# Kernel optimization log

Measured on AMD Instinct MI355X. Metric: run time of the kernel, lower is better.

## Reference

```python
import jax, jax.numpy as jnp
import numpy as np
from jax import lax

EPS = 1e-8


def setup_inputs() -> dict:
    key = jax.random.key(0)
    k1, k2, k3, k4, k5 = jax.random.split(key, 5)
    b, c_in, c_out, h, w_sp, k, z = 8, 256, 256, 128, 128, 3, 512
    return {
        "x": jax.random.normal(k1, (b, c_in, h, w_sp), dtype=jnp.float32),
        "w": jax.random.normal(k2, (b, z), dtype=jnp.float32),
        "weight": jax.random.normal(k3, (c_out, c_in, k, k), dtype=jnp.float32),
        "affine_w": jax.random.normal(k4, (c_in, z), dtype=jnp.float32) * 0.02,
        "affine_b": jax.random.normal(k5, (c_in,), dtype=jnp.float32) * 0.02,
    }


def reference(x, w, weight, affine_w, affine_b):
    # style: [b, c_in] -> broadcast over (out_ch, kh, kw); +1 as in StyleGAN2
    style = w @ affine_w.T + affine_b + 1.0                      # [b, c_in]
    wgt = weight[None] * style[:, None, :, None, None]           # [b, O, I, kh, kw]
    # demodulation
    denom = lax.rsqrt(jnp.sum(wgt * wgt, axis=(2, 3, 4)) + EPS)  # [b, O]
    wgt = wgt * denom[:, :, None, None, None]

    # per-sample conv (equivalent to groups=b grouped conv), 'same' padding
    def conv_one(xi, wi):
        # xi: [I, H, W], wi: [O, I, kh, kw]
        return lax.conv_general_dilated(
            xi[None], wi, window_strides=(1, 1), padding="SAME",
            dimension_numbers=("NCHW", "OIHW", "NCHW"))[0]

    return jax.vmap(conv_one)(x, wgt)                            # [b, O, H, W]
```

## Files before the change

kernel.cpp:

```cpp
#include <hip/hip_runtime.h>
#include <hip/hip_bf16.h>

#define EPS 1e-8f

using short8 = __attribute__((ext_vector_type(8))) short;
using f32x16 = __attribute__((ext_vector_type(16))) float;
typedef unsigned short u16;

#define BARRIER() do { __builtin_amdgcn_s_barrier(); \
                       asm volatile("" ::: "memory"); } while (0)
#define LGKM0() asm volatile("s_waitcnt lgkmcnt(0)" ::: "memory")

__device__ __forceinline__ u16 f2bf(float f) {
    union { float f; unsigned u; } v; v.f = f;
    unsigned u = v.u;
    return (u16)((u + 0x7FFFu + ((u >> 16) & 1u)) >> 16);
}

__global__ void style_kernel(const float* __restrict__ w,
                             const float* __restrict__ affine_w,
                             const float* __restrict__ affine_b,
                             float* __restrict__ style) {
    int b = blockIdx.x;
    int i = threadIdx.x;
    __shared__ float wb[512];
    for (int z = threadIdx.x; z < 512; z += 256) wb[z] = w[b * 512 + z];
    __syncthreads();
    const float* aw = affine_w + i * 512;
    float acc = 0.f;
#pragma unroll 4
    for (int z = 0; z < 512; z += 4) {
        float4 a4 = *reinterpret_cast<const float4*>(aw + z);
        acc += a4.x * wb[z] + a4.y * wb[z + 1] + a4.z * wb[z + 2] + a4.w * wb[z + 3];
    }
    style[b * 256 + i] = acc + affine_b[i] + 1.0f;
}

__global__ void modw_kernel(const float* __restrict__ weight,
                            const float* __restrict__ style,
                            u16* __restrict__ wgt) {
    int b = blockIdx.x >> 8;
    int o = blockIdx.x & 255;
    int ic = threadIdx.x;
    float s = style[b * 256 + ic];
    const float* wp = weight + (size_t)(o * 256 + ic) * 9;
    float m[9];
    float ss = 0.f;
#pragma unroll
    for (int t = 0; t < 9; ++t) { m[t] = wp[t] * s; ss += m[t] * m[t]; }
#pragma unroll
    for (int off = 32; off > 0; off >>= 1) ss += __shfl_down(ss, off);
    __shared__ float part[4];
    int lane = threadIdx.x & 63, wid = threadIdx.x >> 6;
    if (lane == 0) part[wid] = ss;
    __syncthreads();
    float denom = rsqrtf(part[0] + part[1] + part[2] + part[3] + EPS);
    int g = ic >> 3, j = ic & 7;
#pragma unroll
    for (int t = 0; t < 9; ++t) {
        size_t idx = ((((size_t)(b * 9 + t) * 32 + g) * 256 + o) << 3) + j;
        wgt[idx] = f2bf(m[t] * denom);
    }
}

__global__ __launch_bounds__(256, 2) void conv_kernel(
    const float* __restrict__ x,
    const u16* __restrict__ wgt,
    float* __restrict__ out) {

    __shared__ __align__(16) u16 Xs[2][4][4][130][8];

    int bid = blockIdx.x;
    int swz = (bid & 7) * 128 + (bid >> 3);
    int ht = swz & 63, ot = (swz >> 6) & 1, b = swz >> 7;
    int h0 = ht * 2;

    int tid = threadIdx.x, lane = tid & 63, wid = tid >> 6;
    int wm = wid >> 1, wr = wid & 1;
    int l31 = lane & 31, lh = lane >> 5;

    int hr = h0 + wid - 1;
    bool hValid = ((unsigned)hr < 128u);
    int hc = hValid ? hr : 0;

    const u16* aBase = wgt + ((size_t)(b * 9) * 32 * 256 +
                              (size_t)(lh * 256 + ot * 128 + wm * 64 + l31)) * 8;
    const float* xBase = x + ((size_t)(b * 256) * 128 + hc) * 128;

    auto loadA = [&](short8 dst[2][2], int c, int t) {
#pragma unroll
        for (int kk = 0; kk < 2; ++kk)
#pragma unroll
            for (int mi = 0; mi < 2; ++mi)
                dst[kk][mi] = *reinterpret_cast<const short8*>(
                    aBase + (size_t)(((t * 32) + c * 4 + kk * 2) * 256 + mi * 32) * 8);
    };
    auto issueX = [&](float* dst, int c1, int bt) {
        int g = bt >> 1, half = bt & 1;
        const float* sp = xBase + (size_t)(c1 * 32 + g * 8) * 16384 + half * 64 + lane;
#pragma unroll
        for (int j = 0; j < 8; ++j) dst[j] = sp[(size_t)j * 16384];
    };
    auto writeX = [&](const float* src, int bt, int bx) {
        int g = bt >> 1, half = bt & 1;
        union { u16 u[8]; short8 v; } pk;
#pragma unroll
        for (int j = 0; j < 8; ++j) {
            __hip_bfloat16 hb = __float2bfloat16(src[j]);
            pk.u[j] = reinterpret_cast<u16&>(hb);
        }
        *reinterpret_cast<short8*>(&Xs[bx][wid][g][1 + half * 64 + lane][0]) = pk.v;
    };

    {
        short8 z = {0, 0, 0, 0, 0, 0, 0, 0};
        short8* p0 = reinterpret_cast<short8*>(&Xs[0][0][0][0][0]);
        for (int i = tid; i < 4160; i += 256) p0[i] = z;
    }
    __syncthreads();

    short8 afC[2][2], afN[2][2];
    if (hValid) {
        float xg0[8][8];
#pragma unroll
        for (int bt = 0; bt < 8; ++bt) issueX(xg0[bt], 0, bt);
#pragma unroll
        for (int bt = 0; bt < 8; ++bt) writeX(xg0[bt], bt, 0);
    }
    loadA(afC, 0, 0);
    LGKM0();
    BARRIER();

    f32x16 acc[2][4] = {};
    float xg[2][8];

    for (int c = 0; c < 8; ++c) {
        int buf = c & 1;
        bool stage = (c < 7) && hValid;
#pragma unroll
        for (int t = 0; t < 9; ++t) {
            bool lastTap = (c == 7 && t == 8);
            if (!lastTap)
                loadA(afN, t < 8 ? c : c + 1, t < 8 ? t + 1 : 0);
            if (stage) {
                if (t >= 2) writeX(xg[t & 1], t - 2, buf ^ 1);
                if (t < 8)  issueX(xg[t & 1], c + 1, t);
                if (t == 8) writeX(xg[1], 7, buf ^ 1);
            }

            int kh = t / 3, kw = t - kh * 3;
            short8 bx8[2][4];
#pragma unroll
            for (int kk = 0; kk < 2; ++kk)
#pragma unroll
                for (int ni = 0; ni < 4; ++ni)
                    bx8[kk][ni] = *reinterpret_cast<const short8*>(
                        &Xs[buf][wr + kh][kk * 2 + lh][ni * 32 + l31 + kw][0]);
            __builtin_amdgcn_s_setprio(1);
#pragma unroll
            for (int mi = 0; mi < 2; ++mi)
#pragma unroll
                for (int ni = 0; ni < 4; ++ni)
#pragma unroll
                    for (int kk = 0; kk < 2; ++kk)
                        acc[mi][ni] = __builtin_amdgcn_mfma_f32_32x32x16_bf16(
                            afC[kk][mi], bx8[kk][ni], acc[mi][ni], 0, 0, 0);
            __builtin_amdgcn_s_setprio(0);

            if (!lastTap) {
#pragma unroll
                for (int k2 = 0; k2 < 2; ++k2)
#pragma unroll
                    for (int mi = 0; mi < 2; ++mi)
                        afC[k2][mi] = afN[k2][mi];
            }
        }
        if (c < 7) { LGKM0(); BARRIER(); }
    }

    int h = h0 + wr;
#pragma unroll
    for (int mi = 0; mi < 2; ++mi) {
        int ob = ot * 128 + wm * 64 + mi * 32 + 4 * lh;
#pragma unroll
        for (int ni = 0; ni < 4; ++ni) {
            int w_ = ni * 32 + l31;
#pragma unroll
            for (int reg = 0; reg < 16; ++reg) {
                int o = ob + (reg & 3) + 8 * (reg >> 2);
                out[(((size_t)(b * 256 + o) * 128 + h) * 128) + w_] = acc[mi][ni][reg];
            }
        }
    }
}

extern "C" void kernel_launch(void* const* d_in, const int* in_sizes, int n_in,
                              void* d_out, int out_size, void* d_ws, size_t ws_size,
                              hipStream_t stream) {
    const float* x        = (const float*)d_in[0];
    const float* w        = (const float*)d_in[1];
    const float* weight   = (const float*)d_in[2];
    const float* affine_w = (const float*)d_in[3];
    const float* affine_b = (const float*)d_in[4];
    float* out = (float*)d_out;

    float* style = (float*)d_ws;
    u16* wgt = (u16*)((char*)d_ws + 8192);

    style_kernel<<<8, 256, 0, stream>>>(w, affine_w, affine_b, style);
    modw_kernel<<<2048, 256, 0, stream>>>(weight, style, wgt);
    conv_kernel<<<1024, 256, 0, stream>>>(x, wgt, out);
}
```

Baseline: 182.9 us.

## Retile conv blocks to one output row across all 256 output channels

Each block now computes one spatial row for all 256 output channels, where before it computed two rows for 128 channels. The LDS input halo shrinks from 4 rows to 3, and that halo is shared across all output channels. This cuts redundant x loads and fp32-to-bf16 conversions, since the old ot split loaded the same input twice. In exchange, each modulated weight fragment is reused across only one row instead of two, which doubles weight traffic per output, and boundary rows now need per-row validity checks during staging.

```diff
diff --git a/kernel.cpp b/kernel.cpp
--- a/kernel.cpp
+++ b/kernel.cpp
@@ -68,24 +68,17 @@
     const u16* __restrict__ wgt,
     float* __restrict__ out) {
 
-    __shared__ __align__(16) u16 Xs[2][4][4][130][8];
+    __shared__ __align__(16) u16 Xs[2][3][4][130][8];
 
     int bid = blockIdx.x;
     int swz = (bid & 7) * 128 + (bid >> 3);
-    int ht = swz & 63, ot = (swz >> 6) & 1, b = swz >> 7;
-    int h0 = ht * 2;
+    int h = swz & 127, b = swz >> 7;
 
     int tid = threadIdx.x, lane = tid & 63, wid = tid >> 6;
-    int wm = wid >> 1, wr = wid & 1;
     int l31 = lane & 31, lh = lane >> 5;
 
-    int hr = h0 + wid - 1;
-    bool hValid = ((unsigned)hr < 128u);
-    int hc = hValid ? hr : 0;
-
     const u16* aBase = wgt + ((size_t)(b * 9) * 32 * 256 +
-                              (size_t)(lh * 256 + ot * 128 + wm * 64 + l31)) * 8;
-    const float* xBase = x + ((size_t)(b * 256) * 128 + hc) * 128;
+                              (size_t)(lh * 256 + wid * 64 + l31)) * 8;
 
     auto loadA = [&](short8 dst[2][2], int c, int t) {
 #pragma unroll
@@ -95,37 +88,44 @@
                 dst[kk][mi] = *reinterpret_cast<const short8*>(
                     aBase + (size_t)(((t * 32) + c * 4 + kk * 2) * 256 + mi * 32) * 8);
     };
-    auto issueX = [&](float* dst, int c1, int bt) {
-        int g = bt >> 1, half = bt & 1;
-        const float* sp = xBase + (size_t)(c1 * 32 + g * 8) * 16384 + half * 64 + lane;
-#pragma unroll
-        for (int j = 0; j < 8; ++j) dst[j] = sp[(size_t)j * 16384];
+    auto issueX = [&](float* dst, int c1, int u) {
+        int row = u >> 3, g = (u >> 1) & 3, half = u & 1;
+        int hr = h + row - 1;
+        if ((unsigned)hr < 128u) {
+            const float* sp = x + (((size_t)(b * 256 + c1 * 32 + g * 8)) * 128 + hr) * 128 +
+                              half * 64 + lane;
+#pragma unroll
+            for (int j = 0; j < 8; ++j) dst[j] = sp[(size_t)j * 16384];
+        }
     };
-    auto writeX = [&](const float* src, int bt, int bx) {
-        int g = bt >> 1, half = bt & 1;
-        union { u16 u[8]; short8 v; } pk;
-#pragma unroll
-        for (int j = 0; j < 8; ++j) {
-            __hip_bfloat16 hb = __float2bfloat16(src[j]);
-            pk.u[j] = reinterpret_cast<u16&>(hb);
-        }
-        *reinterpret_cast<short8*>(&Xs[bx][wid][g][1 + half * 64 + lane][0]) = pk.v;
+    auto writeX = [&](const float* src, int u, int bx) {
+        int row = u >> 3, g = (u >> 1) & 3, half = u & 1;
+        int hr = h + row - 1;
+        if ((unsigned)hr < 128u) {
+            union { u16 u[8]; short8 v; } pk;
+#pragma unroll
+            for (int j = 0; j < 8; ++j) {
+                __hip_bfloat16 hb = __float2bfloat16(src[j]);
+                pk.u[j] = reinterpret_cast<u16&>(hb);
+            }
+            *reinterpret_cast<short8*>(&Xs[bx][row][g][1 + half * 64 + lane][0]) = pk.v;
+        }
     };
 
     {
         short8 z = {0, 0, 0, 0, 0, 0, 0, 0};
         short8* p0 = reinterpret_cast<short8*>(&Xs[0][0][0][0][0]);
-        for (int i = tid; i < 4160; i += 256) p0[i] = z;
+        for (int i = tid; i < 3120; i += 256) p0[i] = z;
     }
     __syncthreads();
 
     short8 afC[2][2], afN[2][2];
-    if (hValid) {
-        float xg0[8][8];
-#pragma unroll
-        for (int bt = 0; bt < 8; ++bt) issueX(xg0[bt], 0, bt);
-#pragma unroll
-        for (int bt = 0; bt < 8; ++bt) writeX(xg0[bt], bt, 0);
+    {
+        float xg0[6][8];
+#pragma unroll
+        for (int k = 0; k < 6; ++k) issueX(xg0[k], 0, wid * 6 + k);
+#pragma unroll
+        for (int k = 0; k < 6; ++k) writeX(xg0[k], wid * 6 + k, 0);
     }
     loadA(afC, 0, 0);
     LGKM0();
@@ -136,16 +136,15 @@
 
     for (int c = 0; c < 8; ++c) {
         int buf = c & 1;
-        bool stage = (c < 7) && hValid;
+        bool stage = (c < 7);
 #pragma unroll
         for (int t = 0; t < 9; ++t) {
             bool lastTap = (c == 7 && t == 8);
             if (!lastTap)
                 loadA(afN, t < 8 ? c : c + 1, t < 8 ? t + 1 : 0);
             if (stage) {
-                if (t >= 2) writeX(xg[t & 1], t - 2, buf ^ 1);
-                if (t < 8)  issueX(xg[t & 1], c + 1, t);
-                if (t == 8) writeX(xg[1], 7, buf ^ 1);
+                if (t >= 2 && t < 8) writeX(xg[t & 1], wid * 6 + (t - 2), buf ^ 1);
+                if (t < 6)           issueX(xg[t & 1], c + 1, wid * 6 + t);
             }
 
             int kh = t / 3, kw = t - kh * 3;
@@ -155,7 +154,7 @@
 #pragma unroll
                 for (int ni = 0; ni < 4; ++ni)
                     bx8[kk][ni] = *reinterpret_cast<const short8*>(
-                        &Xs[buf][wr + kh][kk * 2 + lh][ni * 32 + l31 + kw][0]);
+                        &Xs[buf][kh][kk * 2 + lh][ni * 32 + l31 + kw][0]);
             __builtin_amdgcn_s_setprio(1);
 #pragma unroll
             for (int mi = 0; mi < 2; ++mi)
@@ -178,10 +177,9 @@
         if (c < 7) { LGKM0(); BARRIER(); }
     }
 
-    int h = h0 + wr;
 #pragma unroll
     for (int mi = 0; mi < 2; ++mi) {
-        int ob = ot * 128 + wm * 64 + mi * 32 + 4 * lh;
+        int ob = wid * 64 + mi * 32 + 4 * lh;
 #pragma unroll
         for (int ni = 0; ni < 4; ++ni) {
             int w_ = ni * 32 + l31;
```

New measurement: 184.5 us. No clear change (+0.9%).
